# Performance work log

Measured on AMD Instinct MI355X. Metric: run time of the kernel, lower is better.

## Reference

```python
import jax, jax.numpy as jnp
import numpy as np

N = 50000      # nodes
E = 800000     # edges
F_IN = 5       # (E, X, Y, Z, T_rel)
D = 128        # hidden_dim
H = 4          # heads
C = D // H     # per-head channels = 32
L = 3          # num_gat_layers
NEG_SLOPE = 0.2


def setup_inputs() -> dict:
    key = jax.random.key(0)
    ks = jax.random.split(key, 20)
    s = 0.05
    inp = {
        "x": jax.random.normal(ks[0], (N, F_IN), dtype=jnp.float32),
        "edge_index": jax.random.randint(ks[1], (2, E), 0, N, dtype=jnp.int32),
        # node encoder
        "enc_W": jax.random.normal(ks[2], (F_IN, D), dtype=jnp.float32) * s,
        "enc_b": jnp.zeros((D,), jnp.float32),
        # stacked GATv2 params for L layers
        "Wl": jax.random.normal(ks[3], (L, D, D), dtype=jnp.float32) * s,
        "bl": jnp.zeros((L, D), jnp.float32),
        "Wr": jax.random.normal(ks[4], (L, D, D), dtype=jnp.float32) * s,
        "br": jnp.zeros((L, D), jnp.float32),
        "att": jax.random.normal(ks[5], (L, H, C), dtype=jnp.float32) * s,
        "gat_bias": jnp.zeros((L, D), jnp.float32),
        # edge classifier MLP (258 -> 128 -> 64 -> 1)
        "c1_W": jax.random.normal(ks[6], (2 * D + 2, D), dtype=jnp.float32) * s,
        "c1_b": jnp.zeros((D,), jnp.float32),
        "c2_W": jax.random.normal(ks[7], (D, 64), dtype=jnp.float32) * s,
        "c2_b": jnp.zeros((64,), jnp.float32),
        "c3_W": jax.random.normal(ks[8], (64, 1), dtype=jnp.float32) * s,
        "c3_b": jnp.zeros((1,), jnp.float32),
    }
    return inp


def _gatv2_layer(h, src, dst, Wl, bl, Wr, br, att, bias):
    # GATv2Conv (PyG semantics, share_weights=False, concat=True, self-loops added)
    xl = (h @ Wl + bl).reshape(N, H, C)   # source transform
    xr = (h @ Wr + br).reshape(N, H, C)   # target transform
    e = jax.nn.leaky_relu(xl[src] + xr[dst], NEG_SLOPE)      # [E', H, C]
    alpha = jnp.einsum("ehc,hc->eh", e, att)                 # [E', H]
    # scatter-softmax over incoming edges of each dst node (numerically stable)
    amax = jax.ops.segment_max(alpha, dst, num_segments=N)
    alpha = jnp.exp(alpha - amax[dst])
    denom = jax.ops.segment_sum(alpha, dst, num_segments=N)
    alpha = alpha / (denom[dst] + 1e-16)
    msg = xl[src] * alpha[:, :, None]                        # [E', H, C]
    out = jax.ops.segment_sum(msg, dst, num_segments=N)      # [N, H, C]
    return out.reshape(N, D) + bias


def reference(x, edge_index, enc_W, enc_b, Wl, bl, Wr, br, att, gat_bias,
              c1_W, c1_b, c2_W, c2_b, c3_W, c3_b):
    h = jax.nn.relu(x @ enc_W + enc_b)
    # add self-loops (PyG GATv2Conv default add_self_loops=True)
    loops = jnp.arange(N, dtype=edge_index.dtype)
    src = jnp.concatenate([edge_index[0], loops])
    dst = jnp.concatenate([edge_index[1], loops])
    for i in range(L):
        h = jax.nn.elu(_gatv2_layer(h, src, dst, Wl[i], bl[i], Wr[i], br[i], att[i], gat_bias[i]))
    # edge feature head on ORIGINAL edges
    row, col = edge_index[0], edge_index[1]
    ni = h[row]                                              # [E, D]
    nj = h[col]                                              # [E, D]
    delta_t = jnp.abs(x[row, 4] - x[col, 4])[:, None]        # [E, 1]
    dist = jnp.sqrt(jnp.sum((x[row, 1:4] - x[col, 1:4]) ** 2, axis=1))[:, None]
    ef = jnp.concatenate([ni, nj, delta_t, dist], axis=1)    # [E, 2D+2]
    o = jax.nn.relu(ef @ c1_W + c1_b)
    o = jax.nn.relu(o @ c2_W + c2_b)
    o = o @ c3_W + c3_b
    return o.reshape(-1)
```

## Files before the change

### kernel.cpp

```cpp
#include <hip/hip_runtime.h>
#include <hip/hip_bf16.h>

#define N_NODES 50000
#define N_EDGES 800000
#define DIM 128
#define NLAYER 3
#define NEG 0.2f

typedef __attribute__((ext_vector_type(8))) short short8;
typedef __attribute__((ext_vector_type(4))) float f32x4;

__global__ __launch_bounds__(256) void zero_kernel(int* p, int n) {
    int i = blockIdx.x * 256 + threadIdx.x;
    if (i < n) p[i] = 0;
}

__global__ __launch_bounds__(256) void hist_kernel(const int* __restrict__ dst, int* __restrict__ counts) {
    int e = blockIdx.x * 256 + threadIdx.x;
    if (e < N_EDGES) atomicAdd(&counts[dst[e]], 1);
}

__global__ __launch_bounds__(256) void scan1_kernel(const int* __restrict__ counts, int* __restrict__ indptr,
                                                    int* __restrict__ bsum, int n) {
    __shared__ int buf[256];
    int t = threadIdx.x;
    int i = blockIdx.x * 256 + t;
    int v = (i < n) ? counts[i] : 0;
    buf[t] = v;
    __syncthreads();
    for (int off = 1; off < 256; off <<= 1) {
        int add = (t >= off) ? buf[t - off] : 0;
        __syncthreads();
        buf[t] += add;
        __syncthreads();
    }
    if (i < n) indptr[i + 1] = buf[t];
    if (t == 255) bsum[blockIdx.x] = buf[255];
}

__global__ __launch_bounds__(256) void scan2_kernel(int* __restrict__ bsum, int* __restrict__ boff,
                                                    int* __restrict__ indptr, int nb) {
    __shared__ int buf[256];
    int t = threadIdx.x;
    int v = (t < nb) ? bsum[t] : 0;
    buf[t] = v;
    __syncthreads();
    for (int off = 1; off < 256; off <<= 1) {
        int add = (t >= off) ? buf[t - off] : 0;
        __syncthreads();
        buf[t] += add;
        __syncthreads();
    }
    if (t < nb) boff[t] = buf[t] - v;
    if (t == 0) indptr[0] = 0;
}

__global__ __launch_bounds__(256) void scan3_kernel(int* __restrict__ indptr, const int* __restrict__ boff, int n) {
    int i = blockIdx.x * 256 + threadIdx.x;
    if (i < n) indptr[i + 1] += boff[i >> 8];
}

__global__ __launch_bounds__(256) void place_kernel(const int* __restrict__ srcp, const int* __restrict__ dstp,
                                                    const int* __restrict__ indptr, int* __restrict__ cursor,
                                                    int* __restrict__ csr_src, int* __restrict__ csr_dst,
                                                    int* __restrict__ csr_eid) {
    int e = blockIdx.x * 256 + threadIdx.x;
    if (e < N_EDGES) {
        int dn = dstp[e];
        int pos = indptr[dn] + atomicAdd(&cursor[dn], 1);
        csr_src[pos] = srcp[e];
        csr_dst[pos] = dn;
        csr_eid[pos] = e;
    }
}

__global__ __launch_bounds__(256) void encoder_kernel(const float* __restrict__ x, const float* __restrict__ W,
                                                      const float* __restrict__ b, float* __restrict__ h) {
    int gid = blockIdx.x * 256 + threadIdx.x;
    int n = gid >> 7, d = gid & 127;
    if (n >= N_NODES) return;
    float acc = b[d];
#pragma unroll
    for (int f = 0; f < 5; f++) acc += x[n * 5 + f] * W[f * DIM + d];
    h[n * DIM + d] = fmaxf(acc, 0.f);
}

__global__ __launch_bounds__(256) void prep_weights_kernel(const float* __restrict__ Wl, const float* __restrict__ Wr,
                                                           const float* __restrict__ c1W,
                                                           unsigned short* __restrict__ wt) {
    int idx = blockIdx.x * 256 + threadIdx.x;
    int m = idx >> 14;
    int r = idx & 16383;
    int n = r >> 7, k = r & 127;
    int L = m >> 1, half = m & 1;
    const float* W;
    if (L < 3) W = (half ? Wr : Wl) + (size_t)L * 16384;
    else W = c1W + (size_t)half * 16384;
    float v = W[k * 128 + n];
    __hip_bfloat16 hb = __float2bfloat16(v);
    float rl = v - __bfloat162float(hb);
    __hip_bfloat16 lb = __float2bfloat16(rl);
    wt[(size_t)m * 32768 + n * 128 + k] = *reinterpret_cast<unsigned short*>(&hb);
    wt[(size_t)m * 32768 + 16384 + n * 128 + k] = *reinterpret_cast<unsigned short*>(&lb);
}

template <bool BF16A, bool BF16B>
__global__ __launch_bounds__(256) void transform_mfma_kernel(const float* __restrict__ h,
                                                             const unsigned short* __restrict__ wtA,
                                                             const float* __restrict__ bA,
                                                             const unsigned short* __restrict__ wtB,
                                                             const float* __restrict__ bB,
                                                             void* __restrict__ outA_, void* __restrict__ outB_) {
    __shared__ __align__(16) char hhi[64 * 256];
    __shared__ __align__(16) char hlo[64 * 256];
    int t = threadIdx.x;
    int l = t & 63, w = t >> 6;
    int n0 = blockIdx.x * 64;
    for (int i = t; i < 64 * 32; i += 256) {
        int row = i >> 5, c4 = (i & 31) * 4;
        int n = n0 + row;
        float4 v = make_float4(0.f, 0.f, 0.f, 0.f);
        if (n < N_NODES) v = *(const float4*)&h[(size_t)n * DIM + c4];
        const float* pv = &v.x;
        unsigned short hi4[4], lo4[4];
#pragma unroll
        for (int q = 0; q < 4; q++) {
            __hip_bfloat16 hb = __float2bfloat16(pv[q]);
            float rl = pv[q] - __bfloat162float(hb);
            __hip_bfloat16 lb = __float2bfloat16(rl);
            hi4[q] = *reinterpret_cast<unsigned short*>(&hb);
            lo4[q] = *reinterpret_cast<unsigned short*>(&lb);
        }
        int addr = (row * 256 + c4 * 2) ^ ((row & 7) << 4);
        *(ushort4*)(hhi + addr) = make_ushort4(hi4[0], hi4[1], hi4[2], hi4[3]);
        *(ushort4*)(hlo + addr) = make_ushort4(lo4[0], lo4[1], lo4[2], lo4[3]);
    }
    __syncthreads();

    int lane_m = l & 15, lane_k8 = l >> 4;

#pragma unroll
    for (int mat = 0; mat < 2; mat++) {
        const short* wthi = (const short*)(mat ? wtB : wtA);
        const short* wtlo = wthi + 16384;
        const float* bias = mat ? bB : bA;
        const bool bfout = mat ? BF16B : BF16A;
        short8 bh[2][4], bl_[2][4];
#pragma unroll
        for (int j = 0; j < 2; j++) {
            int nrow = (w * 2 + j) * 16 + lane_m;
#pragma unroll
            for (int ks = 0; ks < 4; ks++) {
                int ke = ks * 32 + lane_k8 * 8;
                bh[j][ks] = *(const short8*)(wthi + nrow * 128 + ke);
                bl_[j][ks] = *(const short8*)(wtlo + nrow * 128 + ke);
            }
        }
        f32x4 acc[4][2];
#pragma unroll
        for (int mt = 0; mt < 4; mt++)
#pragma unroll
            for (int j = 0; j < 2; j++) acc[mt][j] = (f32x4){0.f, 0.f, 0.f, 0.f};
#pragma unroll
        for (int ks = 0; ks < 4; ks++) {
            int kb = ks * 64 + lane_k8 * 16;
#pragma unroll
            for (int mt = 0; mt < 4; mt++) {
                int arow = mt * 16 + lane_m;
                int aswz = (arow & 7) << 4;
                short8 ahi = *(const short8*)(hhi + ((arow * 256 + kb) ^ aswz));
                short8 alo = *(const short8*)(hlo + ((arow * 256 + kb) ^ aswz));
#pragma unroll
                for (int j = 0; j < 2; j++) {
                    acc[mt][j] = __builtin_amdgcn_mfma_f32_16x16x32_bf16(ahi, bh[j][ks], acc[mt][j], 0, 0, 0);
                    acc[mt][j] = __builtin_amdgcn_mfma_f32_16x16x32_bf16(ahi, bl_[j][ks], acc[mt][j], 0, 0, 0);
                    acc[mt][j] = __builtin_amdgcn_mfma_f32_16x16x32_bf16(alo, bh[j][ks], acc[mt][j], 0, 0, 0);
                }
            }
        }
        void* outp = mat ? outB_ : outA_;
#pragma unroll
        for (int j = 0; j < 2; j++) {
            int col = (w * 2 + j) * 16 + lane_m;
            float bv = bias ? bias[col] : 0.f;
#pragma unroll
            for (int mt = 0; mt < 4; mt++) {
#pragma unroll
                for (int r = 0; r < 4; r++) {
                    int node = n0 + mt * 16 + lane_k8 * 4 + r;
                    if (node < N_NODES) {
                        float v = acc[mt][j][r] + bv;
                        if (bfout) {
                            ((__hip_bfloat16*)outp)[(size_t)node * DIM + col] = __float2bfloat16(v);
                        } else {
                            ((float*)outp)[(size_t)node * DIM + col] = v;
                        }
                    }
                }
            }
        }
    }
}

__device__ __forceinline__ float4 bf4_to_f4(ushort4 u) {
    float4 v;
    v.x = __uint_as_float((unsigned)u.x << 16);
    v.y = __uint_as_float((unsigned)u.y << 16);
    v.z = __uint_as_float((unsigned)u.z << 16);
    v.w = __uint_as_float((unsigned)u.w << 16);
    return v;
}

__global__ __launch_bounds__(256) void gat_edge_kernel(const unsigned short* __restrict__ xl,
                                                       const float* __restrict__ xr,
                                                       const float* __restrict__ att, const float* __restrict__ gbias,
                                                       const int* __restrict__ indptr, const int* __restrict__ csr_src,
                                                       float* __restrict__ h_out) {
    int n = blockIdx.x * 4 + (threadIdx.x >> 6);
    int l = threadIdx.x & 63;
    int half = l >> 5;
    int c0 = (l & 31) * 4;
    float4 xrv = *(const float4*)&xr[(size_t)n * DIM + c0];
    float4 attv = *(const float4*)&att[c0];
    int beg = indptr[n], end = indptr[n + 1];

    float m[4], den[4];
    float4 acc[4];
    {
        float4 v = bf4_to_f4(*(const ushort4*)&xl[(size_t)n * DIM + c0]);
        float z, a;
        z = v.x + xrv.x; z = fmaxf(z, NEG * z); a = z * attv.x;
        z = v.y + xrv.y; z = fmaxf(z, NEG * z); a += z * attv.y;
        z = v.z + xrv.z; z = fmaxf(z, NEG * z); a += z * attv.z;
        z = v.w + xrv.w; z = fmaxf(z, NEG * z); a += z * attv.w;
        a += __shfl_xor(a, 1);
        a += __shfl_xor(a, 2);
        a += __shfl_xor(a, 4);
        if (half == 0) {
            m[0] = a; den[0] = 1.f; acc[0] = v;
        } else {
            m[0] = -3.4e38f; den[0] = 0.f; acc[0] = make_float4(0.f, 0.f, 0.f, 0.f);
        }
#pragma unroll
        for (int c = 1; c < 4; c++) { m[c] = -3.4e38f; den[c] = 0.f; acc[c] = make_float4(0.f, 0.f, 0.f, 0.f); }
    }

    for (int i = beg; i < end; i += 8) {
        int s[4];
        bool val[4];
        float4 v[4];
        float a[4];
#pragma unroll
        for (int c = 0; c < 4; c++) {
            int idx = i + 2 * c + half;
            val[c] = idx < end;
            s[c] = val[c] ? csr_src[idx] : n;
        }
#pragma unroll
        for (int c = 0; c < 4; c++) v[c] = bf4_to_f4(*(const ushort4*)&xl[(size_t)s[c] * DIM + c0]);
#pragma unroll
        for (int c = 0; c < 4; c++) {
            float z, aa;
            z = v[c].x + xrv.x; z = fmaxf(z, NEG * z); aa = z * attv.x;
            z = v[c].y + xrv.y; z = fmaxf(z, NEG * z); aa += z * attv.y;
            z = v[c].z + xrv.z; z = fmaxf(z, NEG * z); aa += z * attv.z;
            z = v[c].w + xrv.w; z = fmaxf(z, NEG * z); aa += z * attv.w;
            a[c] = aa;
        }
#pragma unroll
        for (int off = 1; off <= 4; off <<= 1)
#pragma unroll
            for (int c = 0; c < 4; c++) a[c] += __shfl_xor(a[c], off);
#pragma unroll
        for (int c = 0; c < 4; c++) {
            if (!val[c]) a[c] = -3.4e38f;
            float mn = fmaxf(m[c], a[c]);
            float sc = __expf(m[c] - mn), p = __expf(a[c] - mn);
            den[c] = den[c] * sc + p;
            acc[c].x = acc[c].x * sc + p * v[c].x;
            acc[c].y = acc[c].y * sc + p * v[c].y;
            acc[c].z = acc[c].z * sc + p * v[c].z;
            acc[c].w = acc[c].w * sc + p * v[c].w;
            m[c] = mn;
        }
    }
#pragma unroll
    for (int c = 1; c < 4; c++) {
        float mm = fmaxf(m[0], m[c]);
        float s0 = __expf(m[0] - mm), s1 = __expf(m[c] - mm);
        den[0] = den[0] * s0 + den[c] * s1;
        acc[0].x = acc[0].x * s0 + acc[c].x * s1;
        acc[0].y = acc[0].y * s0 + acc[c].y * s1;
        acc[0].z = acc[0].z * s0 + acc[c].z * s1;
        acc[0].w = acc[0].w * s0 + acc[c].w * s1;
        m[0] = mm;
    }
    {
        float mo = __shfl_xor(m[0], 32);
        float dno = __shfl_xor(den[0], 32);
        float4 ao;
        ao.x = __shfl_xor(acc[0].x, 32);
        ao.y = __shfl_xor(acc[0].y, 32);
        ao.z = __shfl_xor(acc[0].z, 32);
        ao.w = __shfl_xor(acc[0].w, 32);
        float mm = fmaxf(m[0], mo);
        float s0 = __expf(m[0] - mm), s1 = __expf(mo - mm);
        den[0] = den[0] * s0 + dno * s1;
        acc[0].x = acc[0].x * s0 + ao.x * s1;
        acc[0].y = acc[0].y * s0 + ao.y * s1;
        acc[0].z = acc[0].z * s0 + ao.z * s1;
        acc[0].w = acc[0].w * s0 + ao.w * s1;
    }
    if (half == 0) {
        float4 gb = *(const float4*)&gbias[c0];
        float inv = 1.f / (den[0] + 1e-16f);
        float4 o;
        o.x = acc[0].x * inv + gb.x;
        o.y = acc[0].y * inv + gb.y;
        o.z = acc[0].z * inv + gb.z;
        o.w = acc[0].w * inv + gb.w;
        o.x = (o.x > 0.f) ? o.x : __expf(o.x) - 1.f;
        o.y = (o.y > 0.f) ? o.y : __expf(o.y) - 1.f;
        o.z = (o.z > 0.f) ? o.z : __expf(o.z) - 1.f;
        o.w = (o.w > 0.f) ? o.w : __expf(o.w) - 1.f;
        *(float4*)&h_out[(size_t)n * DIM + c0] = o;
    }
}

__global__ __launch_bounds__(256) void edge_mlp_kernel(const unsigned* __restrict__ g1u, const unsigned* __restrict__ g2u,
                                                       const float* __restrict__ x,
                                                       const int* __restrict__ csr_src, const int* __restrict__ csr_dst,
                                                       const int* __restrict__ csr_eid,
                                                       const float* __restrict__ W1tail,
                                                       const float* __restrict__ W2, const float* __restrict__ b2,
                                                       const float* __restrict__ W3, const float* __restrict__ b3,
                                                       float* __restrict__ out, int ntiles) {
    __shared__ __align__(16) char smO1[64 * 256];
    __shared__ float smCw[2][128];
    __shared__ float smPart[4][64];
    __shared__ int rowi[64], coli[64], seid[64];
    __shared__ float sdt[64], sdi[64];
    int t = threadIdx.x;
    int l = t & 63, w = t >> 6;

    if (t < 128) {
        smCw[0][t] = W1tail[t];
        smCw[1][t] = W1tail[128 + t];
    }
    float b3v = b3[0];
    float b2v = b2[w * 16 + (l & 15)];
    float w3v = W3[w * 16 + (l & 15)];
    int koff = (l >> 4) * 16;

    short8 bhi[4], blo[4];
    {
        int nrow = w * 16 + (l & 15);
        int kbase = (l >> 4) * 8;
#pragma unroll
        for (int ks = 0; ks < 4; ks++) {
            int ke = ks * 32 + kbase;
            short8 h8, l8;
#pragma unroll
            for (int q = 0; q < 8; q++) {
                float v = W2[(size_t)(ke + q) * 64 + nrow];
                __hip_bfloat16 hb = __float2bfloat16(v);
                float rl = v - __bfloat162float(hb);
                __hip_bfloat16 lb = __float2bfloat16(rl);
                h8[q] = *reinterpret_cast<short*>(&hb);
                l8[q] = *reinterpret_cast<short*>(&lb);
            }
            bhi[ks] = h8;
            blo[ks] = l8;
        }
    }

    const uint4* g1t = (const uint4*)g1u;
    const uint4* g2t = (const uint4*)g2u;

    for (int tile = blockIdx.x; tile < ntiles; tile += gridDim.x) {
        int p0 = tile * 64;
        __syncthreads();
        if (t < 64) {
            int p = p0 + t;
            int r = csr_src[p], c = csr_dst[p];
            rowi[t] = r; coli[t] = c; seid[t] = csr_eid[p];
            sdt[t] = fabsf(x[r * 5 + 4] - x[c * 5 + 4]);
            float dx = x[r * 5 + 1] - x[c * 5 + 1];
            float dy = x[r * 5 + 2] - x[c * 5 + 2];
            float dz = x[r * 5 + 3] - x[c * 5 + 3];
            sdi[t] = sqrtf(dx * dx + dy * dy + dz * dz);
        }
        __syncthreads();
        for (int idx = t; idx < 64 * 16; idx += 256) {
            int e = idx >> 4, s4 = idx & 15;
            uint4 u1 = g1t[(size_t)rowi[e] * 16 + s4];
            uint4 u2 = g2t[(size_t)coli[e] * 16 + s4];
            float dtv = sdt[e], div = sdi[e];
            unsigned uo[4];
            const unsigned* a1 = &u1.x;
            const unsigned* a2 = &u2.x;
#pragma unroll
            for (int q = 0; q < 4; q++) {
                int d = s4 * 8 + q * 2;
                float lo = __uint_as_float(a1[q] << 16) + __uint_as_float(a2[q] << 16) + dtv * smCw[0][d] + div * smCw[1][d];
                float hi = __uint_as_float(a1[q] & 0xffff0000u) + __uint_as_float(a2[q] & 0xffff0000u) +
                           dtv * smCw[0][d + 1] + div * smCw[1][d + 1];
                lo = fmaxf(lo, 0.f); hi = fmaxf(hi, 0.f);
                __hip_bfloat16 blo16 = __float2bfloat16(lo), bhi16 = __float2bfloat16(hi);
                unsigned short ulo = *reinterpret_cast<unsigned short*>(&blo16);
                unsigned short uhi = *reinterpret_cast<unsigned short*>(&bhi16);
                uo[q] = (unsigned)ulo | ((unsigned)uhi << 16);
            }
            int addr = (e * 256 + s4 * 16) ^ ((e & 7) << 4);
            *(uint4*)(smO1 + addr) = *(uint4*)uo;
        }
        __syncthreads();
        f32x4 acc[4];
#pragma unroll
        for (int mt = 0; mt < 4; mt++) acc[mt] = (f32x4){0.f, 0.f, 0.f, 0.f};
#pragma unroll
        for (int ks = 0; ks < 4; ks++) {
#pragma unroll
            for (int mt = 0; mt < 4; mt++) {
                int mrow = mt * 16 + (l & 15);
                short8 afrag = *(const short8*)(smO1 + ((mrow * 256 + koff + ks * 64) ^ ((mrow & 7) << 4)));
                acc[mt] = __builtin_amdgcn_mfma_f32_16x16x32_bf16(afrag, bhi[ks], acc[mt], 0, 0, 0);
                acc[mt] = __builtin_amdgcn_mfma_f32_16x16x32_bf16(afrag, blo[ks], acc[mt], 0, 0, 0);
            }
        }
        float p[4][4];
#pragma unroll
        for (int mt = 0; mt < 4; mt++)
#pragma unroll
            for (int r = 0; r < 4; r++) p[mt][r] = fmaxf(acc[mt][r] + b2v, 0.f) * w3v;
#pragma unroll
        for (int off = 8; off >= 1; off >>= 1)
#pragma unroll
            for (int mt = 0; mt < 4; mt++)
#pragma unroll
                for (int r = 0; r < 4; r++) p[mt][r] += __shfl_xor(p[mt][r], off);
        if ((l & 15) == 0) {
            int g = l >> 4;
#pragma unroll
            for (int mt = 0; mt < 4; mt++)
#pragma unroll
                for (int r = 0; r < 4; r++) smPart[w][mt * 16 + g * 4 + r] = p[mt][r];
        }
        __syncthreads();
        if (t < 64) out[seid[t]] = smPart[0][t] + smPart[1][t] + smPart[2][t] + smPart[3][t] + b3v;
    }
}

extern "C" void kernel_launch(void* const* d_in, const int* in_sizes, int n_in,
                              void* d_out, int out_size, void* d_ws, size_t ws_size,
                              hipStream_t stream) {
    const float* x = (const float*)d_in[0];
    const int* ei = (const int*)d_in[1];
    const float* enc_W = (const float*)d_in[2];
    const float* enc_b = (const float*)d_in[3];
    const float* Wl = (const float*)d_in[4];
    const float* bl = (const float*)d_in[5];
    const float* Wr = (const float*)d_in[6];
    const float* br = (const float*)d_in[7];
    const float* att = (const float*)d_in[8];
    const float* gbias = (const float*)d_in[9];
    const float* c1_W = (const float*)d_in[10];
    const float* c1_b = (const float*)d_in[11];
    const float* c2_W = (const float*)d_in[12];
    const float* c2_b = (const float*)d_in[13];
    const float* c3_W = (const float*)d_in[14];
    const float* c3_b = (const float*)d_in[15];
    float* out = (float*)d_out;

    float* h = (float*)d_ws;
    float* xl = h + (size_t)N_NODES * DIM;
    float* xr = xl + (size_t)N_NODES * DIM;
    int* csr_src = (int*)(xr + (size_t)N_NODES * DIM);
    int* csr_dst = csr_src + N_EDGES;
    int* csr_eid = csr_dst + N_EDGES;
    int* indptr = csr_eid + N_EDGES;
    int* counts = indptr + (N_NODES + 1);
    int* bsum = counts + N_NODES;
    int* boff = bsum + 256;
    uintptr_t wp = (uintptr_t)(boff + 256);
    wp = (wp + 15) & ~(uintptr_t)15;
    unsigned short* wt = (unsigned short*)wp;

    const int* srcp = ei;
    const int* dstp = ei + N_EDGES;
    const int NB = (N_NODES + 255) / 256;
    const int TGRID = (N_NODES + 63) / 64;

    prep_weights_kernel<<<8 * 16384 / 256, 256, 0, stream>>>(Wl, Wr, c1_W, wt);

    zero_kernel<<<(N_NODES + 255) / 256, 256, 0, stream>>>(counts, N_NODES);
    hist_kernel<<<N_EDGES / 256, 256, 0, stream>>>(dstp, counts);
    scan1_kernel<<<NB, 256, 0, stream>>>(counts, indptr, bsum, N_NODES);
    scan2_kernel<<<1, 256, 0, stream>>>(bsum, boff, indptr, NB);
    scan3_kernel<<<NB, 256, 0, stream>>>(indptr, boff, N_NODES);
    zero_kernel<<<(N_NODES + 255) / 256, 256, 0, stream>>>(counts, N_NODES);
    place_kernel<<<N_EDGES / 256, 256, 0, stream>>>(srcp, dstp, indptr, counts, csr_src, csr_dst, csr_eid);

    encoder_kernel<<<(N_NODES * DIM) / 256, 256, 0, stream>>>(x, enc_W, enc_b, h);

    for (int i = 0; i < NLAYER; i++) {
        transform_mfma_kernel<true, false><<<TGRID, 256, 0, stream>>>(
            h, wt + (size_t)(i * 2) * 32768, bl + (size_t)i * DIM,
            wt + (size_t)(i * 2 + 1) * 32768, br + (size_t)i * DIM, xl, xr);
        gat_edge_kernel<<<N_NODES / 4, 256, 0, stream>>>((const unsigned short*)xl, xr,
                                                         att + (size_t)i * DIM,
                                                         gbias + (size_t)i * DIM, indptr, csr_src, h);
    }

    transform_mfma_kernel<true, true><<<TGRID, 256, 0, stream>>>(
        h, wt + (size_t)6 * 32768, c1_b, wt + (size_t)7 * 32768, nullptr, xl, xr);

    edge_mlp_kernel<<<1280, 256, 0, stream>>>((const unsigned*)xl, (const unsigned*)xr, x,
                                              csr_src, csr_dst, csr_eid, c1_W + 256 * DIM,
                                              c2_W, c2_b, c3_W, c3_b, out, N_EDGES / 64);
}
```

Measured before the change: 532.1 us.

## Store xr in bf16, fold counter zeroing into existing kernels, widen edge MLP grid

The target-side transform xr is now written as bf16 instead of fp32 and converted back to float in the GAT edge kernel, which halves its write and read traffic per layer. The two zero_kernel launches are removed: the counters are cleared inside prep_weights and again inside scan1 after they are read. The edge MLP grid grows from 1280 to 2048 blocks. The cost is lower precision in the attention logits that use xr.

```diff
diff --git a/kernel.cpp b/kernel.cpp
--- a/kernel.cpp
+++ b/kernel.cpp
@@ -10,17 +10,12 @@
 typedef __attribute__((ext_vector_type(8))) short short8;
 typedef __attribute__((ext_vector_type(4))) float f32x4;
 
-__global__ __launch_bounds__(256) void zero_kernel(int* p, int n) {
-    int i = blockIdx.x * 256 + threadIdx.x;
-    if (i < n) p[i] = 0;
-}
-
 __global__ __launch_bounds__(256) void hist_kernel(const int* __restrict__ dst, int* __restrict__ counts) {
     int e = blockIdx.x * 256 + threadIdx.x;
     if (e < N_EDGES) atomicAdd(&counts[dst[e]], 1);
 }
 
-__global__ __launch_bounds__(256) void scan1_kernel(const int* __restrict__ counts, int* __restrict__ indptr,
+__global__ __launch_bounds__(256) void scan1_kernel(int* __restrict__ counts, int* __restrict__ indptr,
                                                     int* __restrict__ bsum, int n) {
     __shared__ int buf[256];
     int t = threadIdx.x;
@@ -34,7 +29,10 @@
         buf[t] += add;
         __syncthreads();
     }
-    if (i < n) indptr[i + 1] = buf[t];
+    if (i < n) {
+        indptr[i + 1] = buf[t];
+        counts[i] = 0;
+    }
     if (t == 255) bsum[blockIdx.x] = buf[255];
 }
 
@@ -87,8 +85,10 @@
 
 __global__ __launch_bounds__(256) void prep_weights_kernel(const float* __restrict__ Wl, const float* __restrict__ Wr,
                                                            const float* __restrict__ c1W,
-                                                           unsigned short* __restrict__ wt) {
+                                                           unsigned short* __restrict__ wt,
+                                                           int* __restrict__ counts) {
     int idx = blockIdx.x * 256 + threadIdx.x;
+    if (idx < N_NODES) counts[idx] = 0;
     int m = idx >> 14;
     int r = idx & 16383;
     int n = r >> 7, k = r & 127;
@@ -104,13 +104,13 @@
     wt[(size_t)m * 32768 + 16384 + n * 128 + k] = *reinterpret_cast<unsigned short*>(&lb);
 }
 
-template <bool BF16A, bool BF16B>
 __global__ __launch_bounds__(256) void transform_mfma_kernel(const float* __restrict__ h,
                                                              const unsigned short* __restrict__ wtA,
                                                              const float* __restrict__ bA,
                                                              const unsigned short* __restrict__ wtB,
                                                              const float* __restrict__ bB,
-                                                             void* __restrict__ outA_, void* __restrict__ outB_) {
+                                                             __hip_bfloat16* __restrict__ outA,
+                                                             __hip_bfloat16* __restrict__ outB) {
     __shared__ __align__(16) char hhi[64 * 256];
     __shared__ __align__(16) char hlo[64 * 256];
     int t = threadIdx.x;
@@ -144,7 +144,6 @@
         const short* wthi = (const short*)(mat ? wtB : wtA);
         const short* wtlo = wthi + 16384;
         const float* bias = mat ? bB : bA;
-        const bool bfout = mat ? BF16B : BF16A;
         short8 bh[2][4], bl_[2][4];
 #pragma unroll
         for (int j = 0; j < 2; j++) {
@@ -178,7 +177,7 @@
                 }
             }
         }
-        void* outp = mat ? outB_ : outA_;
+        __hip_bfloat16* outp = mat ? outB : outA;
 #pragma unroll
         for (int j = 0; j < 2; j++) {
             int col = (w * 2 + j) * 16 + lane_m;
@@ -189,12 +188,7 @@
                 for (int r = 0; r < 4; r++) {
                     int node = n0 + mt * 16 + lane_k8 * 4 + r;
                     if (node < N_NODES) {
-                        float v = acc[mt][j][r] + bv;
-                        if (bfout) {
-                            ((__hip_bfloat16*)outp)[(size_t)node * DIM + col] = __float2bfloat16(v);
-                        } else {
-                            ((float*)outp)[(size_t)node * DIM + col] = v;
-                        }
+                        outp[(size_t)node * DIM + col] = __float2bfloat16(acc[mt][j][r] + bv);
                     }
                 }
             }
@@ -212,7 +206,7 @@
 }
 
 __global__ __launch_bounds__(256) void gat_edge_kernel(const unsigned short* __restrict__ xl,
-                                                       const float* __restrict__ xr,
+                                                       const unsigned short* __restrict__ xr,
                                                        const float* __restrict__ att, const float* __restrict__ gbias,
                                                        const int* __restrict__ indptr, const int* __restrict__ csr_src,
                                                        float* __restrict__ h_out) {
@@ -220,7 +214,7 @@
     int l = threadIdx.x & 63;
     int half = l >> 5;
     int c0 = (l & 31) * 4;
-    float4 xrv = *(const float4*)&xr[(size_t)n * DIM + c0];
+    float4 xrv = bf4_to_f4(*(const ushort4*)&xr[(size_t)n * DIM + c0]);
     float4 attv = *(const float4*)&att[c0];
     int beg = indptr[n], end = indptr[n + 1];
 
@@ -473,8 +467,8 @@
     float* out = (float*)d_out;
 
     float* h = (float*)d_ws;
-    float* xl = h + (size_t)N_NODES * DIM;
-    float* xr = xl + (size_t)N_NODES * DIM;
+    __hip_bfloat16* xl = (__hip_bfloat16*)(h + (size_t)N_NODES * DIM);
+    __hip_bfloat16* xr = xl + (size_t)N_NODES * DIM;
     int* csr_src = (int*)(xr + (size_t)N_NODES * DIM);
     int* csr_dst = csr_src + N_EDGES;
     int* csr_eid = csr_dst + N_EDGES;
@@ -491,31 +485,29 @@
     const int NB = (N_NODES + 255) / 256;
     const int TGRID = (N_NODES + 63) / 64;
 
-    prep_weights_kernel<<<8 * 16384 / 256, 256, 0, stream>>>(Wl, Wr, c1_W, wt);
-
-    zero_kernel<<<(N_NODES + 255) / 256, 256, 0, stream>>>(counts, N_NODES);
+    prep_weights_kernel<<<8 * 16384 / 256, 256, 0, stream>>>(Wl, Wr, c1_W, wt, counts);
+
     hist_kernel<<<N_EDGES / 256, 256, 0, stream>>>(dstp, counts);
     scan1_kernel<<<NB, 256, 0, stream>>>(counts, indptr, bsum, N_NODES);
     scan2_kernel<<<1, 256, 0, stream>>>(bsum, boff, indptr, NB);
     scan3_kernel<<<NB, 256, 0, stream>>>(indptr, boff, N_NODES);
-    zero_kernel<<<(N_NODES + 255) / 256, 256, 0, stream>>>(counts, N_NODES);
     place_kernel<<<N_EDGES / 256, 256, 0, stream>>>(srcp, dstp, indptr, counts, csr_src, csr_dst, csr_eid);
 
     encoder_kernel<<<(N_NODES * DIM) / 256, 256, 0, stream>>>(x, enc_W, enc_b, h);
 
     for (int i = 0; i < NLAYER; i++) {
-        transform_mfma_kernel<true, false><<<TGRID, 256, 0, stream>>>(
+        transform_mfma_kernel<<<TGRID, 256, 0, stream>>>(
             h, wt + (size_t)(i * 2) * 32768, bl + (size_t)i * DIM,
             wt + (size_t)(i * 2 + 1) * 32768, br + (size_t)i * DIM, xl, xr);
-        gat_edge_kernel<<<N_NODES / 4, 256, 0, stream>>>((const unsigned short*)xl, xr,
+        gat_edge_kernel<<<N_NODES / 4, 256, 0, stream>>>((const unsigned short*)xl, (const unsigned short*)xr,
                                                          att + (size_t)i * DIM,
                                                          gbias + (size_t)i * DIM, indptr, csr_src, h);
     }
 
-    transform_mfma_kernel<true, true><<<TGRID, 256, 0, stream>>>(
+    transform_mfma_kernel<<<TGRID, 256, 0, stream>>>(
         h, wt + (size_t)6 * 32768, c1_b, wt + (size_t)7 * 32768, nullptr, xl, xr);
 
-    edge_mlp_kernel<<<1280, 256, 0, stream>>>((const unsigned*)xl, (const unsigned*)xr, x,
+    edge_mlp_kernel<<<2048, 256, 0, stream>>>((const unsigned*)xl, (const unsigned*)xr, x,
                                               csr_src, csr_dst, csr_eid, c1_W + 256 * DIM,
                                               c2_W, c2_b, c3_W, c3_b, out, N_EDGES / 64);
 }
```

Result: no change. 525.1 us (-1.3%).
